# Kernel optimization log

Hardware: AMD Instinct MI355X
Metric: run time of the kernel (lower is better)

## Reference

```python
import jax, jax.numpy as jnp
import numpy as np

N = 10  # input_size
P = 6   # part_num


def setup_inputs() -> dict:
    key = jax.random.key(0)
    X = jax.random.uniform(key, (N,), dtype=jnp.float32)
    # Learned params as initialized in __init__ (cast to float32)
    a = jnp.tile(jnp.linspace(0.0, 1.0, P, dtype=jnp.float32)[None, :], (N, 1))  # [N,P]
    b = jnp.full((N, P), 1.0 / P ** 1.5, dtype=jnp.float32)                       # [N,P]
    y = jnp.full((P ** (N - 1), P), 0.5, dtype=jnp.float32)                       # rule consequents
    return {"X": X, "a": a, "b": b, "y": y}


def reference(X, a, b, y):
    # Gaussian memberships, one row per input feature: [N, P]
    h_ = jnp.exp(-((a - X[:, None]) ** 2) / (2.0 * b ** 2))
    # Sequential outer-product chain over the N feature rows -> flat [P**N]
    h = h_[0]
    for i in range(1, N):  # fixed trace-time loop over feature dim (N is a hyperparam)
        h = (h[:, None] * h_[i][None, :]).reshape(-1)
    # Weighted average of rule consequents (scalar)
    num = jnp.sum(h * y.reshape(-1))
    den = jnp.sum(h)
    return num / den
```

## Files before the change

kernel.cpp:

```cpp
#include <hip/hip_runtime.h>
#include <math.h>


#define NF 10
#define PP 6
#define HI 7776
#define HI4 1944
#define BLK 256
#define ROWS 2

typedef float fvec4 __attribute__((ext_vector_type(4)));


__device__ __forceinline__ float memb(const float* X, const float* a,
                                      const float* b, int idx) {
    const int k = idx / PP;
    const float d = a[idx] - X[k];
    const float bb = b[idx];
    return __expf(-(d * d) / (2.0f * bb * bb));
}

__global__ __launch_bounds__(BLK) void tsk_fused(const float* __restrict__ X,
                                                 const float* __restrict__ a,
                                                 const float* __restrict__ b,
                                                 const float* __restrict__ y,
                                                 float* __restrict__ ws) {
    __shared__ float h[NF][PP];
    __shared__ float wlo[HI];
    __shared__ float ssum[BLK / 64][ROWS];
    const int t = threadIdx.x;

    if (t < NF * PP) h[t / PP][t % PP] = memb(X, a, b, t);
    __syncthreads();

    for (int c = t; c < HI; c += BLK) {
        int u = c;
        const int d9 = u % 6; u /= 6;
        const int d8 = u % 6; u /= 6;
        const int d7 = u % 6; u /= 6;
        const int d6 = u % 6; u /= 6;
        const int d5 = u;
        wlo[c] = h[5][d5] * h[6][d6] * h[7][d7] * h[8][d8] * h[9][d9];
    }
    __syncthreads();

    const fvec4* __restrict__ wlo4 = (const fvec4*)wlo;
    const int r0 = blockIdx.x * ROWS;

    float accs[ROWS];
    for (int i = 0; i < ROWS; ++i) {
        const fvec4* __restrict__ yrow = (const fvec4*)(y + (size_t)(r0 + i) * HI);
        float acc = 0.0f;
        #pragma unroll
        for (int k = 0; k < 7; ++k) {
            const int c = t + k * BLK;
            const fvec4 yv = __builtin_nontemporal_load(yrow + c);
            const fvec4 wv = wlo4[c];
            acc += yv.x * wv.x + yv.y * wv.y + yv.z * wv.z + yv.w * wv.w;
        }
        const int c = t + 7 * BLK;
        if (c < HI4) {
            const fvec4 yv = __builtin_nontemporal_load(yrow + c);
            const fvec4 wv = wlo4[c];
            acc += yv.x * wv.x + yv.y * wv.y + yv.z * wv.z + yv.w * wv.w;
        }
        accs[i] = acc;
    }

    #pragma unroll
    for (int i = 0; i < ROWS; ++i) {
        #pragma unroll
        for (int off = 32; off > 0; off >>= 1)
            accs[i] += __shfl_down(accs[i], off, 64);
    }
    const int lane = t & 63;
    const int wave = t >> 6;
    if (lane == 0) {
        #pragma unroll
        for (int i = 0; i < ROWS; ++i) ssum[wave][i] = accs[i];
    }
    __syncthreads();
    if (t < ROWS) {
        float s = 0.0f;
        #pragma unroll
        for (int w = 0; w < BLK / 64; ++w) s += ssum[w][t];
        int u = r0 + t;
        const int d4 = u % 6; u /= 6;
        const int d3 = u % 6; u /= 6;
        const int d2 = u % 6; u /= 6;
        const int d1 = u % 6; u /= 6;
        const int d0 = u;
        const float whi = h[0][d0] * h[1][d1] * h[2][d2] * h[3][d3] * h[4][d4];
        ws[r0 + t] = s * whi;
    }
}

__global__ __launch_bounds__(1024) void tsk_reduce(const float* __restrict__ X,
                                                   const float* __restrict__ a,
                                                   const float* __restrict__ b,
                                                   const float* __restrict__ ws,
                                                   float* __restrict__ out) {
    __shared__ float h[NF * PP];
    __shared__ float ssum[16];
    const int t = threadIdx.x;
    if (t < NF * PP) h[t] = memb(X, a, b, t);

    float acc = 0.0f;
    #pragma unroll
    for (int k = 0; k < 8; ++k) {
        const int r = t + k * 1024;
        if (r < HI) acc += ws[r];
    }
    #pragma unroll
    for (int off = 32; off > 0; off >>= 1) acc += __shfl_down(acc, off, 64);
    const int lane = t & 63;
    const int wave = t >> 6;
    if (lane == 0) ssum[wave] = acc;
    __syncthreads();
    if (t == 0) {
        float num = 0.0f;
        #pragma unroll
        for (int w = 0; w < 16; ++w) num += ssum[w];
        float den = 1.0f;
        for (int k = 0; k < NF; ++k) {
            float s = 0.0f;
            for (int i = 0; i < PP; ++i) s += h[k * PP + i];
            den *= s;
        }
        out[0] = num / den;
    }
}

extern "C" void kernel_launch(void* const* d_in, const int* in_sizes, int n_in,
                              void* d_out, int out_size, void* d_ws, size_t ws_size,
                              hipStream_t stream) {
    const float* X = (const float*)d_in[0];
    const float* a = (const float*)d_in[1];
    const float* b = (const float*)d_in[2];
    const float* y = (const float*)d_in[3];
    float* out = (float*)d_out;
    float* ws  = (float*)d_ws;

    tsk_fused<<<HI / ROWS, BLK, 0, stream>>>(X, a, b, y, ws);
    tsk_reduce<<<1, 1024, 0, stream>>>(X, a, b, ws, out);
}
```

Baseline: 312.3 us.

## Process four y rows per block with interleaved loads and staged wlo build

Each block now handles four rows of y instead of two. The four rows' loads are interleaved in a single loop so each shared-memory wlo vector is read once and reused across all rows, and more global loads are in flight per thread. The per-block table of 7776 low-order membership products is now built in stages through shared scratch arrays instead of per-element div/mod chains. This halves the number of blocks that rebuild the table, at the cost of more registers, an extra ~6KB of LDS, and extra barriers.

```diff
diff --git a/kernel.cpp b/kernel.cpp
--- a/kernel.cpp
+++ b/kernel.cpp
@@ -7,7 +7,7 @@
 #define HI 7776
 #define HI4 1944
 #define BLK 256
-#define ROWS 2
+#define ROWS 4
 
 typedef float fvec4 __attribute__((ext_vector_type(4)));
 
@@ -27,57 +27,72 @@
                                                  float* __restrict__ ws) {
     __shared__ float h[NF][PP];
     __shared__ float wlo[HI];
+    __shared__ float scr[1296 + 216];
     __shared__ float ssum[BLK / 64][ROWS];
     const int t = threadIdx.x;
+    float* __restrict__ A = scr;
+    float* __restrict__ B = scr + 1296;
 
     if (t < NF * PP) h[t / PP][t % PP] = memb(X, a, b, t);
     __syncthreads();
 
-    for (int c = t; c < HI; c += BLK) {
-        int u = c;
-        const int d9 = u % 6; u /= 6;
-        const int d8 = u % 6; u /= 6;
-        const int d7 = u % 6; u /= 6;
-        const int d6 = u % 6; u /= 6;
-        const int d5 = u;
-        wlo[c] = h[5][d5] * h[6][d6] * h[7][d7] * h[8][d8] * h[9][d9];
-    }
+    if (t < 36)  A[t] = h[5][t / 6] * h[6][t % 6];
+    __syncthreads();
+    if (t < 216) B[t] = A[t / 6] * h[7][t % 6];
+    __syncthreads();
+    for (int c = t; c < 1296; c += BLK) A[c] = B[c / 6] * h[8][c % 6];
+    __syncthreads();
+    for (int c = t; c < HI; c += BLK)  wlo[c] = A[c / 6] * h[9][c % 6];
     __syncthreads();
 
     const fvec4* __restrict__ wlo4 = (const fvec4*)wlo;
     const int r0 = blockIdx.x * ROWS;
+    const fvec4* __restrict__ yr0 = (const fvec4*)(y + (size_t)(r0 + 0) * HI);
+    const fvec4* __restrict__ yr1 = (const fvec4*)(y + (size_t)(r0 + 1) * HI);
+    const fvec4* __restrict__ yr2 = (const fvec4*)(y + (size_t)(r0 + 2) * HI);
+    const fvec4* __restrict__ yr3 = (const fvec4*)(y + (size_t)(r0 + 3) * HI);
 
-    float accs[ROWS];
-    for (int i = 0; i < ROWS; ++i) {
-        const fvec4* __restrict__ yrow = (const fvec4*)(y + (size_t)(r0 + i) * HI);
-        float acc = 0.0f;
-        #pragma unroll
-        for (int k = 0; k < 7; ++k) {
-            const int c = t + k * BLK;
-            const fvec4 yv = __builtin_nontemporal_load(yrow + c);
-            const fvec4 wv = wlo4[c];
-            acc += yv.x * wv.x + yv.y * wv.y + yv.z * wv.z + yv.w * wv.w;
-        }
+    float acc0 = 0.f, acc1 = 0.f, acc2 = 0.f, acc3 = 0.f;
+    #pragma unroll
+    for (int k = 0; k < 7; ++k) {
+        const int c = t + k * BLK;
+        const fvec4 wv = wlo4[c];
+        const fvec4 y0 = __builtin_nontemporal_load(yr0 + c);
+        const fvec4 y1 = __builtin_nontemporal_load(yr1 + c);
+        const fvec4 y2 = __builtin_nontemporal_load(yr2 + c);
+        const fvec4 y3 = __builtin_nontemporal_load(yr3 + c);
+        acc0 += y0.x * wv.x + y0.y * wv.y + y0.z * wv.z + y0.w * wv.w;
+        acc1 += y1.x * wv.x + y1.y * wv.y + y1.z * wv.z + y1.w * wv.w;
+        acc2 += y2.x * wv.x + y2.y * wv.y + y2.z * wv.z + y2.w * wv.w;
+        acc3 += y3.x * wv.x + y3.y * wv.y + y3.z * wv.z + y3.w * wv.w;
+    }
+    {
         const int c = t + 7 * BLK;
         if (c < HI4) {
-            const fvec4 yv = __builtin_nontemporal_load(yrow + c);
             const fvec4 wv = wlo4[c];
-            acc += yv.x * wv.x + yv.y * wv.y + yv.z * wv.z + yv.w * wv.w;
+            const fvec4 y0 = __builtin_nontemporal_load(yr0 + c);
+            const fvec4 y1 = __builtin_nontemporal_load(yr1 + c);
+            const fvec4 y2 = __builtin_nontemporal_load(yr2 + c);
+            const fvec4 y3 = __builtin_nontemporal_load(yr3 + c);
+            acc0 += y0.x * wv.x + y0.y * wv.y + y0.z * wv.z + y0.w * wv.w;
+            acc1 += y1.x * wv.x + y1.y * wv.y + y1.z * wv.z + y1.w * wv.w;
+            acc2 += y2.x * wv.x + y2.y * wv.y + y2.z * wv.z + y2.w * wv.w;
+            acc3 += y3.x * wv.x + y3.y * wv.y + y3.z * wv.z + y3.w * wv.w;
         }
-        accs[i] = acc;
     }
 
     #pragma unroll
-    for (int i = 0; i < ROWS; ++i) {
-        #pragma unroll
-        for (int off = 32; off > 0; off >>= 1)
-            accs[i] += __shfl_down(accs[i], off, 64);
+    for (int off = 32; off > 0; off >>= 1) {
+        acc0 += __shfl_down(acc0, off, 64);
+        acc1 += __shfl_down(acc1, off, 64);
+        acc2 += __shfl_down(acc2, off, 64);
+        acc3 += __shfl_down(acc3, off, 64);
     }
     const int lane = t & 63;
     const int wave = t >> 6;
     if (lane == 0) {
-        #pragma unroll
-        for (int i = 0; i < ROWS; ++i) ssum[wave][i] = accs[i];
+        ssum[wave][0] = acc0; ssum[wave][1] = acc1;
+        ssum[wave][2] = acc2; ssum[wave][3] = acc3;
     }
     __syncthreads();
     if (t < ROWS) {
```

Result: no change. 311.3 us (-0.3%).
